# Kernel tuning notes

Hardware: AMD Instinct MI355X
Metric: run time of the kernel (lower is better)

Reference implementation:

```python
import jax, jax.numpy as jnp
import numpy as np

N, E, F, H, R, NB, G, C = 100000, 500000, 128, 64, 16, 30, 1000, 10


def setup_inputs() -> dict:
    key = jax.random.key(0)
    ks = jax.random.split(key, 12)
    s = 0.05
    x = jax.random.normal(ks[0], (N, F), jnp.float32)
    edge_index = jax.random.randint(ks[1], (2, E), 0, N, dtype=jnp.int32)
    edge_norm = jax.random.uniform(ks[2], (E,), jnp.float32)
    edge_type = jax.random.randint(ks[3], (E,), 0, R, dtype=jnp.int32)
    seq_lengths = jnp.full((G,), N // G, dtype=jnp.int32)  # 1000 graphs x 100 nodes
    return dict(
        x=x, edge_index=edge_index, edge_norm=edge_norm, edge_type=edge_type,
        seq_lengths=seq_lengths, avec=0,
        w1_rel=jax.random.normal(ks[4], (F, H), jnp.float32) * s,
        w1_root=jax.random.normal(ks[5], (F, H), jnp.float32) * s,
        b1=jnp.zeros((H,), jnp.float32),
        bases=jax.random.normal(ks[6], (NB, H, H), jnp.float32) * s,
        comp=jax.random.normal(ks[7], (R, NB), jnp.float32) * s,
        w2_root=jax.random.normal(ks[8], (H, H), jnp.float32) * s,
        b2=jnp.zeros((H,), jnp.float32),
        lin_w=jax.random.normal(ks[9], (2 * (F + H), H), jnp.float32) * s,
        lin_b=jnp.zeros((H,), jnp.float32),
        fc_w=jax.random.normal(ks[10], (H, C), jnp.float32) * s,
        fc_b=jnp.zeros((C,), jnp.float32),
    )


def reference(x, edge_index, edge_norm, edge_type, seq_lengths, avec,
              w1_rel, w1_root, b1, bases, comp, w2_root, b2,
              lin_w, lin_b, fc_w, fc_b):
    src, dst = edge_index[0], edge_index[1]

    # --- GraphConv (PyG): out_i = W_rel @ sum_{j->i} w_ji x_j + W_root x_i + b
    msg = x[src] * edge_norm[:, None]                       # [E, F]
    agg = jax.ops.segment_sum(msg, dst, num_segments=N)     # [N, F]
    h = agg @ w1_rel + x @ w1_root + b1                     # [N, H]

    # --- RGCNConv with basis decomposition, mean aggregation per relation
    W = jnp.einsum('rb,bio->rio', comp, bases)              # [R, H, H]
    hs = h[src]                                             # [E, H]
    out = h @ w2_root + b2                                  # root transform + bias
    for r in range(R):  # small fixed relation count
        m = (edge_type == r).astype(h.dtype)                # [E]
        s_r = jax.ops.segment_sum(hs * m[:, None], dst, num_segments=N)
        c_r = jax.ops.segment_sum(m, dst, num_segments=N)
        out = out + (s_r / jnp.maximum(c_r, 1.0)[:, None]) @ W[r]

    feats = jnp.concatenate([x, out], axis=-1)              # [N, F+H]

    # --- ragged per-graph sum & max pooling (replaces the Python loop)
    bounds = jnp.cumsum(seq_lengths)
    gid = jnp.searchsorted(bounds, jnp.arange(N), side='right')  # [N] graph ids
    gsum = jax.ops.segment_sum(feats, gid, num_segments=G)       # [G, F+H]
    gmax = jax.ops.segment_max(feats, gid, num_segments=G)       # [G, F+H]

    hidden = jax.nn.relu(jnp.concatenate([gsum, gmax], -1) @ lin_w + lin_b)
    # dropout is identity at inference
    logits = hidden @ fc_w + fc_b                           # [G, C]
    if avec:
        return logits
    return jax.nn.log_softmax(logits, -1)
```

## Files before the change

### kernel.cpp

```cpp
#include <hip/hip_runtime.h>
#include <hip/hip_bf16.h>

#define NN 100000
#define NE 500000
#define FD 128
#define HD 64
#define RR 16
#define NBASE 30
#define GG 1000
#define CC 10
#define NGROUP 6250

typedef __attribute__((ext_vector_type(8))) short bf16x8;
typedef __attribute__((ext_vector_type(4))) float f32x4;

__device__ inline unsigned short f2b(float x) {
  __hip_bfloat16 b = __float2bfloat16(x);
  return *reinterpret_cast<unsigned short*>(&b);
}
__device__ inline float b2f(unsigned short u) {
  return __uint_as_float(((unsigned)u) << 16);
}

__global__ void k_basis(const float* comp, const float* bases, unsigned short* Wt) {
  int idx = blockIdx.x * 256 + threadIdx.x;
  int r = idx >> 12, kj = idx & 4095;
  int k = kj >> 6, n = kj & 63;
  float acc = 0.0f;
  for (int b = 0; b < NBASE; ++b)
    acc += comp[r * NBASE + b] * bases[b * 4096 + kj];
  Wt[(r << 12) + n * 64 + k] = f2b(acc);
}

__global__ void k_wcvt(const float* w_root, const float* w_rel, const float* w2,
                       unsigned short* wcat, unsigned short* w2t) {
  int idx = blockIdx.x * 256 + threadIdx.x;
  if (idx < 16384) {
    int n = idx >> 7, k = idx & 127;
    float v = (n < 64) ? w_root[k * 64 + n] : w_rel[k * 64 + (n - 64)];
    wcat[n * 128 + k] = f2b(v);
  } else if (idx < 16384 + 4096) {
    int i2 = idx - 16384;
    int n = i2 >> 6, k = i2 & 63;
    w2t[n * 64 + k] = f2b(w2[k * 64 + n]);
  }
}

__global__ __launch_bounds__(256) void k_proj_mfma(const float* x, const unsigned short* wcat,
                                                   const float* b1, unsigned short* hroot_bf,
                                                   unsigned short* xw_bf) {
  __shared__ float red[4][64][33];
  __shared__ float ldsH[16][68];
  __shared__ unsigned short ldsX[16][72];
  int wv = threadIdx.x >> 6, l = threadIdx.x & 63, m = l & 15, q = l >> 4;
  int n0 = blockIdx.x * 16;
  const float* xr = x + (size_t)(n0 + m) * FD + wv * 32 + q * 8;
  float4 xa = *reinterpret_cast<const float4*>(xr);
  float4 xb = *reinterpret_cast<const float4*>(xr + 4);
  bf16x8 a;
  a[0] = (short)f2b(xa.x); a[1] = (short)f2b(xa.y);
  a[2] = (short)f2b(xa.z); a[3] = (short)f2b(xa.w);
  a[4] = (short)f2b(xb.x); a[5] = (short)f2b(xb.y);
  a[6] = (short)f2b(xb.z); a[7] = (short)f2b(xb.w);
  f32x4 zero = {0.0f, 0.0f, 0.0f, 0.0f};
#pragma unroll
  for (int nt = 0; nt < 8; ++nt) {
    bf16x8 b = *reinterpret_cast<const bf16x8*>(wcat + (nt * 16 + m) * 128 + wv * 32 + q * 8);
    f32x4 acc = __builtin_amdgcn_mfma_f32_16x16x32_bf16(a, b, zero, 0, 0, 0);
#pragma unroll
    for (int i = 0; i < 4; ++i) red[wv][l][nt * 4 + i] = acc[i];
  }
  __syncthreads();
#pragma unroll
  for (int t2 = 0; t2 < 2; ++t2) {
    int nt = wv * 2 + t2;
    float s0 = 0, s1 = 0, s2 = 0, s3 = 0;
#pragma unroll
    for (int w = 0; w < 4; ++w) {
      s0 += red[w][l][nt * 4 + 0];
      s1 += red[w][l][nt * 4 + 1];
      s2 += red[w][l][nt * 4 + 2];
      s3 += red[w][l][nt * 4 + 3];
    }
    if (nt < 4) {
      float bb = b1[nt * 16 + m];
      ldsH[q * 4 + 0][nt * 16 + m] = s0 + bb;
      ldsH[q * 4 + 1][nt * 16 + m] = s1 + bb;
      ldsH[q * 4 + 2][nt * 16 + m] = s2 + bb;
      ldsH[q * 4 + 3][nt * 16 + m] = s3 + bb;
    } else {
      int cc = (nt - 4) * 16 + m;
      ldsX[q * 4 + 0][cc] = f2b(s0);
      ldsX[q * 4 + 1][cc] = f2b(s1);
      ldsX[q * 4 + 2][cc] = f2b(s2);
      ldsX[q * 4 + 3][cc] = f2b(s3);
    }
  }
  __syncthreads();
  int t = threadIdx.x;
  {
    int row = t >> 4, c4 = (t & 15) * 4;
    ushort4 o;
    o.x = f2b(ldsH[row][c4 + 0]);
    o.y = f2b(ldsH[row][c4 + 1]);
    o.z = f2b(ldsH[row][c4 + 2]);
    o.w = f2b(ldsH[row][c4 + 3]);
    *reinterpret_cast<ushort4*>(&hroot_bf[(size_t)(n0 + row) * 64 + c4]) = o;
  }
  if (t < 128) {
    int row = t >> 3, c8 = (t & 7) * 8;
    uint4 v = *reinterpret_cast<const uint4*>(&ldsX[row][c8]);
    *reinterpret_cast<uint4*>(&xw_bf[(size_t)(n0 + row) * 64 + c8]) = v;
  }
}

__global__ void k_hists(const int* ei, const int* etype, int* hist1, int* hist2) {
  __shared__ int lh[RR];
  if (threadIdx.x < RR) lh[threadIdx.x] = 0;
  __syncthreads();
  for (int e = blockIdx.x * 256 + threadIdx.x; e < NE; e += gridDim.x * 256) {
    int t = etype[e];
    atomicAdd(&lh[t], 1);
    atomicAdd(&hist2[ei[NE + e] * RR + t], 1);
  }
  __syncthreads();
  if (threadIdx.x < RR) atomicAdd(&hist1[threadIdx.x], lh[threadIdx.x]);
}

__global__ void k_scan1(const int* hist1, int* offs, int* ctr1) {
  if (threadIdx.x == 0) {
    int s = 0;
    for (int r = 0; r < RR; ++r) { offs[r] = s; ctr1[r] = s; s += hist1[r]; }
    offs[RR] = s;
  }
}

__global__ void k_perm1(const int* etype, int* ctr1, int* perm1) {
  __shared__ int lcnt[RR], lbase[RR];
  if (threadIdx.x < RR) lcnt[threadIdx.x] = 0;
  __syncthreads();
  int e = blockIdx.x * 256 + threadIdx.x;
  int t = 0, rank = 0;
  bool valid = e < NE;
  if (valid) { t = etype[e]; rank = atomicAdd(&lcnt[t], 1); }
  __syncthreads();
  if (threadIdx.x < RR) {
    int n = lcnt[threadIdx.x];
    lbase[threadIdx.x] = n ? atomicAdd(&ctr1[threadIdx.x], n) : 0;
  }
  __syncthreads();
  if (valid) perm1[lbase[t] + rank] = e;
}

__device__ inline int block_scan_incl(int v, int* ps, int t) {
  ps[t] = v;
  __syncthreads();
  for (int off = 1; off < 256; off <<= 1) {
    int u = (t >= off) ? ps[t - off] : 0;
    __syncthreads();
    ps[t] += u;
    __syncthreads();
  }
  return ps[t];
}

__global__ void k_scanA(const int* hist2, int* bsum) {
  __shared__ int red[256];
  int t = threadIdx.x;
  red[t] = hist2[blockIdx.x * 256 + t];
  __syncthreads();
  for (int s = 128; s; s >>= 1) {
    if (t < s) red[t] += red[t + s];
    __syncthreads();
  }
  if (t == 0) bsum[blockIdx.x] = red[0];
}

__global__ void k_scanB(int* bsum) {
  int t = threadIdx.x;
  int loc[25];
  int s = 0;
  if (t < 250) {
    for (int i = 0; i < 25; ++i) { loc[i] = bsum[t * 25 + i]; s += loc[i]; }
  }
  __shared__ int ps[256];
  int incl = block_scan_incl(s, ps, t);
  int base = incl - s;
  if (t < 250) {
    int run = base;
    for (int i = 0; i < 25; ++i) { int tmp = loc[i]; bsum[t * 25 + i] = run; run += tmp; }
  }
}

__global__ void k_scanC(const int* hist2, const int* bsum, int* rowptr2, int* ctr2) {
  int t = threadIdx.x;
  int gid = blockIdx.x * 256 + t;
  int v = hist2[gid];
  __shared__ int ps[256];
  int incl = block_scan_incl(v, ps, t);
  int ex = bsum[blockIdx.x] + incl - v;
  rowptr2[gid] = ex;
  ctr2[gid] = ex;
}

__global__ void k_perm2(const int* perm1, const int* ei, const int* etype, const float* enorm,
                        int* ctr2, int* pos2, int* es, float* en) {
  int p = blockIdx.x * 256 + threadIdx.x;
  if (p >= NE) return;
  int e = perm1[p];
  int key = ei[NE + e] * RR + etype[e];
  int pos = atomicAdd(&ctr2[key], 1);
  pos2[p] = pos;
  es[pos] = ei[e];
  en[pos] = enorm[e];
}

__global__ __launch_bounds__(256) void k_gconv_seg(const int* rowptr2, const int* es,
    const float* en, const unsigned short* xw_bf, const unsigned short* hroot_bf,
    unsigned short* h_bf) {
  int wv = threadIdx.x >> 6, l = threadIdx.x & 63;
  int c4 = l & 15, eq = l >> 4;
  int dst = blockIdx.x * 4 + wv;
  int lo = rowptr2[dst * RR];
  int hi = (dst == NN - 1) ? NE : rowptr2[(dst + 1) * RR];
  float4 acc = {0.0f, 0.0f, 0.0f, 0.0f};
  for (int base0 = lo; base0 < hi; base0 += 64) {
    int n = min(64, hi - base0);
    int sv = 0;
    float nv = 0.0f;
    if (l < n) { sv = es[base0 + l]; nv = en[base0 + l]; }
    int k4max = (n + 3) >> 2;
    for (int k4 = 0; k4 < k4max; ++k4) {
      int eid = k4 * 4 + eq;
      int s = __shfl(sv, eid);
      float w = __shfl(nv, eid);
      if (eid < n) {
        uint2 v = *reinterpret_cast<const uint2*>(xw_bf + (size_t)s * 64 + c4 * 4);
        acc.x += b2f((unsigned short)(v.x & 0xffffu)) * w;
        acc.y += b2f((unsigned short)(v.x >> 16)) * w;
        acc.z += b2f((unsigned short)(v.y & 0xffffu)) * w;
        acc.w += b2f((unsigned short)(v.y >> 16)) * w;
      }
    }
  }
  acc.x += __shfl_xor(acc.x, 16); acc.y += __shfl_xor(acc.y, 16);
  acc.z += __shfl_xor(acc.z, 16); acc.w += __shfl_xor(acc.w, 16);
  acc.x += __shfl_xor(acc.x, 32); acc.y += __shfl_xor(acc.y, 32);
  acc.z += __shfl_xor(acc.z, 32); acc.w += __shfl_xor(acc.w, 32);
  if (l < 16) {
    uint2 hb = *reinterpret_cast<const uint2*>(hroot_bf + (size_t)dst * 64 + l * 4);
    acc.x += b2f((unsigned short)(hb.x & 0xffffu));
    acc.y += b2f((unsigned short)(hb.x >> 16));
    acc.z += b2f((unsigned short)(hb.y & 0xffffu));
    acc.w += b2f((unsigned short)(hb.y >> 16));
    ushort4 o;
    o.x = f2b(acc.x); o.y = f2b(acc.y); o.z = f2b(acc.z); o.w = f2b(acc.w);
    *reinterpret_cast<ushort4*>(h_bf + (size_t)dst * 64 + l * 4) = o;
  }
}

__global__ __launch_bounds__(256) void k_root2_mfma(const unsigned short* h_bf,
    const unsigned short* w2t, const float* b2, float* out) {
  int wv = threadIdx.x >> 6, l = threadIdx.x & 63, m = l & 15, q = l >> 4;
  int g = blockIdx.x * 4 + wv;
  if (g >= NGROUP) return;
  int n0 = g * 16;
  f32x4 acc[4];
#pragma unroll
  for (int nt = 0; nt < 4; ++nt) acc[nt] = (f32x4){0, 0, 0, 0};
#pragma unroll
  for (int s = 0; s < 2; ++s) {
    bf16x8 a = *reinterpret_cast<const bf16x8*>(h_bf + (size_t)(n0 + m) * 64 + s * 32 + q * 8);
#pragma unroll
    for (int nt = 0; nt < 4; ++nt) {
      bf16x8 b = *reinterpret_cast<const bf16x8*>(w2t + (nt * 16 + m) * 64 + s * 32 + q * 8);
      acc[nt] = __builtin_amdgcn_mfma_f32_16x16x32_bf16(a, b, acc[nt], 0, 0, 0);
    }
  }
  float b2v[4];
#pragma unroll
  for (int nt = 0; nt < 4; ++nt) b2v[nt] = b2[nt * 16 + m];
#pragma unroll
  for (int i = 0; i < 4; ++i) {
    size_t row = n0 + q * 4 + i;
#pragma unroll
    for (int nt = 0; nt < 4; ++nt)
      out[row * 64 + nt * 16 + m] = acc[nt][i] + b2v[nt];
  }
}

__global__ __launch_bounds__(256) void k_rgcn_y(const int* perm1, const int* ei,
    const int* offs, const int* pos2, const unsigned short* h_bf, const unsigned short* Wt,
    const int* hist2, unsigned short* y_bf) {
  int r = blockIdx.x;
  int lo = offs[r], hi = offs[r + 1];
  int cnt = hi - lo;
  int wv = threadIdx.x >> 6;
  int l = threadIdx.x & 63;
  int m = l & 15, q = l >> 4;
  int ngroups = (cnt + 15) / 16;
  const unsigned short* Wr = Wt + (r << 12);
  bf16x8 bfr[2][4];
#pragma unroll
  for (int s = 0; s < 2; ++s)
#pragma unroll
    for (int nt = 0; nt < 4; ++nt)
      bfr[s][nt] = *reinterpret_cast<const bf16x8*>(Wr + (nt * 16 + m) * 64 + s * 32 + q * 8);

  for (int g = blockIdx.y * 4 + wv; g < ngroups; g += gridDim.y * 4) {
    int base = lo + g * 16;
    int ne = min(16, hi - base);
    int p = base + ((m < ne) ? m : 0);
    int ed = perm1[p];
    int src = ei[ed];
    int dst = ei[NE + ed];
    int pos = pos2[p];
    float inv = 1.0f / (float)max(hist2[dst * RR + r], 1);
    f32x4 acc[4];
#pragma unroll
    for (int nt = 0; nt < 4; ++nt) acc[nt] = (f32x4){0, 0, 0, 0};
    const unsigned short* hrow = h_bf + (size_t)src * 64 + q * 8;
#pragma unroll
    for (int s = 0; s < 2; ++s) {
      bf16x8 afr = *reinterpret_cast<const bf16x8*>(hrow + s * 32);
#pragma unroll
      for (int nt = 0; nt < 4; ++nt)
        acc[nt] = __builtin_amdgcn_mfma_f32_16x16x32_bf16(afr, bfr[s][nt], acc[nt], 0, 0, 0);
    }
#pragma unroll
    for (int i = 0; i < 4; ++i) {
      int row = q * 4 + i;
      float ir = __shfl(inv, row);
      int pr = __shfl(pos, row);
      if (row < ne) {
#pragma unroll
        for (int nt = 0; nt < 4; ++nt)
          y_bf[(size_t)pr * 64 + nt * 16 + m] = f2b(acc[nt][i] * ir);
      }
    }
  }
}

__global__ __launch_bounds__(256) void k_ysum(const int* rowptr2, const unsigned short* y_bf,
                                              float* out) {
  int wv = threadIdx.x >> 6, l = threadIdx.x & 63;
  int c4 = l & 15, eq = l >> 4;
  int dst = blockIdx.x * 4 + wv;
  int lo = rowptr2[dst * RR];
  int hi = (dst == NN - 1) ? NE : rowptr2[(dst + 1) * RR];
  float4 acc = {0.0f, 0.0f, 0.0f, 0.0f};
  for (int row = lo + eq; row < hi; row += 4) {
    uint2 v = *reinterpret_cast<const uint2*>(y_bf + (size_t)row * 64 + c4 * 4);
    acc.x += b2f((unsigned short)(v.x & 0xffffu));
    acc.y += b2f((unsigned short)(v.x >> 16));
    acc.z += b2f((unsigned short)(v.y & 0xffffu));
    acc.w += b2f((unsigned short)(v.y >> 16));
  }
  acc.x += __shfl_xor(acc.x, 16); acc.y += __shfl_xor(acc.y, 16);
  acc.z += __shfl_xor(acc.z, 16); acc.w += __shfl_xor(acc.w, 16);
  acc.x += __shfl_xor(acc.x, 32); acc.y += __shfl_xor(acc.y, 32);
  acc.z += __shfl_xor(acc.z, 32); acc.w += __shfl_xor(acc.w, 32);
  if (l < 16) {
    float4* op = reinterpret_cast<float4*>(out + (size_t)dst * 64 + l * 4);
    float4 o = *op;
    o.x += acc.x; o.y += acc.y; o.z += acc.z; o.w += acc.w;
    *op = o;
  }
}

__global__ void k_bounds(const int* seq, int* bounds) {
  __shared__ int s[GG];
  for (int i = threadIdx.x; i < GG; i += 256) s[i] = seq[i];
  __syncthreads();
  if (threadIdx.x == 0) {
    int acc = 0;
    for (int g = 0; g < GG; ++g) { acc += s[g]; bounds[g] = acc; }
  }
}

__global__ __launch_bounds__(256) void k_head(const float* x, const float* outn,
    const int* bounds, const float* lin_w, const float* lin_b,
    const float* fc_w, const float* fc_b, float* dout) {
  __shared__ float4 psum[5][48], pmax[5][48];
  __shared__ float gsum[192], gmax[192];
  __shared__ float part[4][64];
  __shared__ float hid[HD], lg[CC], mred[2];
  int g = blockIdx.x, t = threadIdx.x;
  int lo = (g == 0) ? 0 : bounds[g - 1];
  int hi = bounds[g];
  int nn = hi - lo;
  if (t < 240) {
    int c4 = t % 48, ch = t / 48;
    int a = lo + (nn * ch) / 5, b = lo + (nn * (ch + 1)) / 5;
    float4 s = {0, 0, 0, 0};
    float4 mx = {-3.4e38f, -3.4e38f, -3.4e38f, -3.4e38f};
    const float* bp;
    int stride;
    if (c4 < 32) { bp = x + (size_t)a * FD + c4 * 4; stride = FD; }
    else         { bp = outn + (size_t)a * 64 + (c4 - 32) * 4; stride = 64; }
    int n = a;
    for (; n + 4 <= b; n += 4) {
      float4 v0 = *reinterpret_cast<const float4*>(bp);
      float4 v1 = *reinterpret_cast<const float4*>(bp + stride);
      float4 v2 = *reinterpret_cast<const float4*>(bp + 2 * stride);
      float4 v3 = *reinterpret_cast<const float4*>(bp + 3 * stride);
      bp += 4 * stride;
      s.x += v0.x + v1.x + v2.x + v3.x;
      s.y += v0.y + v1.y + v2.y + v3.y;
      s.z += v0.z + v1.z + v2.z + v3.z;
      s.w += v0.w + v1.w + v2.w + v3.w;
      mx.x = fmaxf(fmaxf(fmaxf(mx.x, v0.x), fmaxf(v1.x, v2.x)), v3.x);
      mx.y = fmaxf(fmaxf(fmaxf(mx.y, v0.y), fmaxf(v1.y, v2.y)), v3.y);
      mx.z = fmaxf(fmaxf(fmaxf(mx.z, v0.z), fmaxf(v1.z, v2.z)), v3.z);
      mx.w = fmaxf(fmaxf(fmaxf(mx.w, v0.w), fmaxf(v1.w, v2.w)), v3.w);
    }
    for (; n < b; ++n) {
      float4 v = *reinterpret_cast<const float4*>(bp);
      bp += stride;
      s.x += v.x; s.y += v.y; s.z += v.z; s.w += v.w;
      mx.x = fmaxf(mx.x, v.x); mx.y = fmaxf(mx.y, v.y);
      mx.z = fmaxf(mx.z, v.z); mx.w = fmaxf(mx.w, v.w);
    }
    psum[ch][c4] = s;
    pmax[ch][c4] = mx;
  }
  __syncthreads();
  if (t < 48) {
    float4 s = psum[0][t], m = pmax[0][t];
#pragma unroll
    for (int ch = 1; ch < 5; ++ch) {
      float4 ps = psum[ch][t], pm = pmax[ch][t];
      s.x += ps.x; s.y += ps.y; s.z += ps.z; s.w += ps.w;
      m.x = fmaxf(m.x, pm.x); m.y = fmaxf(m.y, pm.y);
      m.z = fmaxf(m.z, pm.z); m.w = fmaxf(m.w, pm.w);
    }
    gsum[t * 4 + 0] = s.x; gsum[t * 4 + 1] = s.y;
    gsum[t * 4 + 2] = s.z; gsum[t * 4 + 3] = s.w;
    gmax[t * 4 + 0] = m.x; gmax[t * 4 + 1] = m.y;
    gmax[t * 4 + 2] = m.z; gmax[t * 4 + 3] = m.w;
  }
  __syncthreads();
  {
    int o = t & 63, pp = t >> 6;
    float a = 0.0f;
    int k0 = pp * 96;
    for (int k = k0; k < k0 + 96; ++k) {
      float gv = (k < 192) ? gsum[k] : gmax[k - 192];
      a += gv * lin_w[k * 64 + o];
    }
    part[pp][o] = a;
  }
  __syncthreads();
  if (t < HD) {
    float a = lin_b[t] + part[0][t] + part[1][t] + part[2][t] + part[3][t];
    hid[t] = fmaxf(a, 0.0f);
  }
  __syncthreads();
  if (t < CC) {
    float a = fc_b[t];
    for (int k = 0; k < HD; ++k) a += hid[k] * fc_w[k * CC + t];
    lg[t] = a;
  }
  __syncthreads();
  if (t == 0) {
    float mm = lg[0];
#pragma unroll
    for (int i = 1; i < CC; ++i) mm = fmaxf(mm, lg[i]);
    float se = 0.0f;
#pragma unroll
    for (int i = 0; i < CC; ++i) se += __expf(lg[i] - mm);
    mred[0] = mm;
    mred[1] = __logf(se);
  }
  __syncthreads();
  if (t < CC) dout[g * CC + t] = lg[t] - mred[0] - mred[1];
}

extern "C" void kernel_launch(void* const* d_in, const int* in_sizes, int n_in,
                              void* d_out, int out_size, void* d_ws, size_t ws_size,
                              hipStream_t stream) {
  const float* x     = (const float*)d_in[0];
  const int* ei      = (const int*)d_in[1];
  const float* enorm = (const float*)d_in[2];
  const int* etype   = (const int*)d_in[3];
  const int* seq     = (const int*)d_in[4];
  const float* w1_rel  = (const float*)d_in[6];
  const float* w1_root = (const float*)d_in[7];
  const float* b1      = (const float*)d_in[8];
  const float* bases   = (const float*)d_in[9];
  const float* comp    = (const float*)d_in[10];
  const float* w2      = (const float*)d_in[11];
  const float* b2      = (const float*)d_in[12];
  const float* lin_w   = (const float*)d_in[13];
  const float* lin_b   = (const float*)d_in[14];
  const float* fc_w    = (const float*)d_in[15];
  const float* fc_b    = (const float*)d_in[16];
  float* dout = (float*)d_out;

  char* p = (char*)d_ws;
  unsigned short* hroot_bf = (unsigned short*)p; p += (size_t)NN * 64 * 2;
  unsigned short* xw_bf    = (unsigned short*)p; p += (size_t)NN * 64 * 2;
  float* out  = (float*)p;  p += (size_t)NN * 64 * 4;
  unsigned short* y_bf = (unsigned short*)p; p += (size_t)NE * 64 * 2;
  unsigned short* h_bf = (unsigned short*)p; p += (size_t)NN * 64 * 2;
  unsigned short* Wt   = (unsigned short*)p; p += (size_t)RR * 4096 * 2;
  unsigned short* wcat = (unsigned short*)p; p += (size_t)128 * 128 * 2;
  unsigned short* w2t  = (unsigned short*)p; p += (size_t)64 * 64 * 2;
  int* perm1   = (int*)p; p += (size_t)NE * 4;
  int* pos2    = (int*)p; p += (size_t)NE * 4;
  int* es      = (int*)p; p += (size_t)NE * 4;
  float* en    = (float*)p; p += (size_t)NE * 4;
  int* hist2   = (int*)p; p += (size_t)NN * RR * 4;
  int* rowptr2 = (int*)p; p += (size_t)NN * RR * 4;
  int* bsum    = (int*)p; p += (size_t)NGROUP * 4;
  int* hist1   = (int*)p; p += 64;
  int* ctr1    = (int*)p; p += 64;
  int* offs    = (int*)p; p += 68;
  int* bounds  = (int*)p; p += (size_t)GG * 4;
  int* ctr2    = (int*)out;

  hipMemsetAsync(hist2, 0, (size_t)NN * RR * 4, stream);
  hipMemsetAsync(hist1, 0, 128, stream);

  hipLaunchKernelGGL(k_basis, dim3(256), dim3(256), 0, stream, comp, bases, Wt);
  hipLaunchKernelGGL(k_wcvt, dim3(80), dim3(256), 0, stream, w1_root, w1_rel, w2, wcat, w2t);
  hipLaunchKernelGGL(k_proj_mfma, dim3(NGROUP), dim3(256), 0, stream, x, wcat, b1,
                     hroot_bf, xw_bf);
  hipLaunchKernelGGL(k_hists, dim3(512), dim3(256), 0, stream, ei, etype, hist1, hist2);
  hipLaunchKernelGGL(k_scan1, dim3(1), dim3(64), 0, stream, hist1, offs, ctr1);
  hipLaunchKernelGGL(k_perm1, dim3((NE + 255) / 256), dim3(256), 0, stream, etype, ctr1, perm1);
  hipLaunchKernelGGL(k_scanA, dim3(NGROUP), dim3(256), 0, stream, hist2, bsum);
  hipLaunchKernelGGL(k_scanB, dim3(1), dim3(256), 0, stream, bsum);
  hipLaunchKernelGGL(k_scanC, dim3(NGROUP), dim3(256), 0, stream, hist2, bsum, rowptr2, ctr2);
  hipLaunchKernelGGL(k_perm2, dim3((NE + 255) / 256), dim3(256), 0, stream,
                     perm1, ei, etype, enorm, ctr2, pos2, es, en);
  hipLaunchKernelGGL(k_gconv_seg, dim3(NN / 4), dim3(256), 0, stream,
                     rowptr2, es, en, xw_bf, hroot_bf, h_bf);
  hipLaunchKernelGGL(k_root2_mfma, dim3((NGROUP + 3) / 4), dim3(256), 0, stream,
                     h_bf, w2t, b2, out);
  hipLaunchKernelGGL(k_rgcn_y, dim3(RR, 128), dim3(256), 0, stream,
                     perm1, ei, offs, pos2, h_bf, Wt, hist2, y_bf);
  hipLaunchKernelGGL(k_ysum, dim3(NN / 4), dim3(256), 0, stream, rowptr2, y_bf, out);
  hipLaunchKernelGGL(k_bounds, dim3(1), dim3(256), 0, stream, seq, bounds);
  hipLaunchKernelGGL(k_head, dim3(GG), dim3(256), 0, stream, x, out, bounds,
                     lin_w, lin_b, fc_w, fc_b, dout);
}
```

Before: 391.5 us.

## Fuse root transform into y-sum, precompute edge src/inv, restructure projection GEMM

Merges the separate root-GEMM kernel into the per-destination y-sum kernel, so the output is written once instead of written and then read-modify-written. The edge permutation kernel now stores each edge's source and inverse relation count in permuted order, which removes the dependent gathers in the RGCN message kernel. The input projection is reworked so each wave does the full K loop for its own 16-row tile with accumulators kept in registers, dropping the cross-wave LDS reduction. The cost is more per-wave register pressure and two extra edge arrays to write.

```diff
diff --git a/kernel.cpp b/kernel.cpp
--- a/kernel.cpp
+++ b/kernel.cpp
@@ -49,68 +49,54 @@
 __global__ __launch_bounds__(256) void k_proj_mfma(const float* x, const unsigned short* wcat,
                                                    const float* b1, unsigned short* hroot_bf,
                                                    unsigned short* xw_bf) {
-  __shared__ float red[4][64][33];
-  __shared__ float ldsH[16][68];
-  __shared__ unsigned short ldsX[16][72];
+  __shared__ unsigned short ldsO[4][16][72];
   int wv = threadIdx.x >> 6, l = threadIdx.x & 63, m = l & 15, q = l >> 4;
-  int n0 = blockIdx.x * 16;
-  const float* xr = x + (size_t)(n0 + m) * FD + wv * 32 + q * 8;
-  float4 xa = *reinterpret_cast<const float4*>(xr);
-  float4 xb = *reinterpret_cast<const float4*>(xr + 4);
-  bf16x8 a;
-  a[0] = (short)f2b(xa.x); a[1] = (short)f2b(xa.y);
-  a[2] = (short)f2b(xa.z); a[3] = (short)f2b(xa.w);
-  a[4] = (short)f2b(xb.x); a[5] = (short)f2b(xb.y);
-  a[6] = (short)f2b(xb.z); a[7] = (short)f2b(xb.w);
-  f32x4 zero = {0.0f, 0.0f, 0.0f, 0.0f};
-#pragma unroll
-  for (int nt = 0; nt < 8; ++nt) {
-    bf16x8 b = *reinterpret_cast<const bf16x8*>(wcat + (nt * 16 + m) * 128 + wv * 32 + q * 8);
-    f32x4 acc = __builtin_amdgcn_mfma_f32_16x16x32_bf16(a, b, zero, 0, 0, 0);
-#pragma unroll
-    for (int i = 0; i < 4; ++i) red[wv][l][nt * 4 + i] = acc[i];
-  }
-  __syncthreads();
-#pragma unroll
-  for (int t2 = 0; t2 < 2; ++t2) {
-    int nt = wv * 2 + t2;
-    float s0 = 0, s1 = 0, s2 = 0, s3 = 0;
-#pragma unroll
-    for (int w = 0; w < 4; ++w) {
-      s0 += red[w][l][nt * 4 + 0];
-      s1 += red[w][l][nt * 4 + 1];
-      s2 += red[w][l][nt * 4 + 2];
-      s3 += red[w][l][nt * 4 + 3];
-    }
-    if (nt < 4) {
-      float bb = b1[nt * 16 + m];
-      ldsH[q * 4 + 0][nt * 16 + m] = s0 + bb;
-      ldsH[q * 4 + 1][nt * 16 + m] = s1 + bb;
-      ldsH[q * 4 + 2][nt * 16 + m] = s2 + bb;
-      ldsH[q * 4 + 3][nt * 16 + m] = s3 + bb;
-    } else {
-      int cc = (nt - 4) * 16 + m;
-      ldsX[q * 4 + 0][cc] = f2b(s0);
-      ldsX[q * 4 + 1][cc] = f2b(s1);
-      ldsX[q * 4 + 2][cc] = f2b(s2);
-      ldsX[q * 4 + 3][cc] = f2b(s3);
-    }
-  }
-  __syncthreads();
-  int t = threadIdx.x;
-  {
-    int row = t >> 4, c4 = (t & 15) * 4;
-    ushort4 o;
-    o.x = f2b(ldsH[row][c4 + 0]);
-    o.y = f2b(ldsH[row][c4 + 1]);
-    o.z = f2b(ldsH[row][c4 + 2]);
-    o.w = f2b(ldsH[row][c4 + 3]);
-    *reinterpret_cast<ushort4*>(&hroot_bf[(size_t)(n0 + row) * 64 + c4]) = o;
-  }
-  if (t < 128) {
-    int row = t >> 3, c8 = (t & 7) * 8;
-    uint4 v = *reinterpret_cast<const uint4*>(&ldsX[row][c8]);
-    *reinterpret_cast<uint4*>(&xw_bf[(size_t)(n0 + row) * 64 + c8]) = v;
+  int g = blockIdx.x * 4 + wv;
+  bool act = g < NGROUP;
+  size_t n0 = (size_t)g * 16;
+  f32x4 acc[8];
+#pragma unroll
+  for (int nt = 0; nt < 8; ++nt) acc[nt] = (f32x4){0, 0, 0, 0};
+  if (act) {
+#pragma unroll
+    for (int s = 0; s < 4; ++s) {
+      const float* xr = x + (n0 + m) * FD + s * 32 + q * 8;
+      float4 xa = *reinterpret_cast<const float4*>(xr);
+      float4 xb = *reinterpret_cast<const float4*>(xr + 4);
+      bf16x8 a;
+      a[0] = (short)f2b(xa.x); a[1] = (short)f2b(xa.y);
+      a[2] = (short)f2b(xa.z); a[3] = (short)f2b(xa.w);
+      a[4] = (short)f2b(xb.x); a[5] = (short)f2b(xb.y);
+      a[6] = (short)f2b(xb.z); a[7] = (short)f2b(xb.w);
+#pragma unroll
+      for (int nt = 0; nt < 8; ++nt) {
+        bf16x8 b = *reinterpret_cast<const bf16x8*>(wcat + (nt * 16 + m) * 128 + s * 32 + q * 8);
+        acc[nt] = __builtin_amdgcn_mfma_f32_16x16x32_bf16(a, b, acc[nt], 0, 0, 0);
+      }
+    }
+  }
+  float b1v[4];
+#pragma unroll
+  for (int nt = 0; nt < 4; ++nt) b1v[nt] = b1[nt * 16 + m];
+#pragma unroll
+  for (int half = 0; half < 2; ++half) {
+#pragma unroll
+    for (int nt = 0; nt < 4; ++nt)
+#pragma unroll
+      for (int i = 0; i < 4; ++i) {
+        float v = acc[half * 4 + nt][i] + (half == 0 ? b1v[nt] : 0.0f);
+        ldsO[wv][q * 4 + i][nt * 16 + m] = f2b(v);
+      }
+    __syncthreads();
+    unsigned short* dstbuf = half == 0 ? hroot_bf : xw_bf;
+#pragma unroll
+    for (int h2 = 0; h2 < 2; ++h2) {
+      int row = h2 * 8 + (l >> 3), ch = l & 7;
+      uint4 v = *reinterpret_cast<const uint4*>(&ldsO[wv][row][ch * 8]);
+      if (act)
+        *reinterpret_cast<uint4*>(&dstbuf[(n0 + row) * 64 + ch * 8]) = v;
+    }
+    __syncthreads();
   }
 }
 
@@ -204,15 +190,19 @@
 }
 
 __global__ void k_perm2(const int* perm1, const int* ei, const int* etype, const float* enorm,
-                        int* ctr2, int* pos2, int* es, float* en) {
+                        const int* hist2, int* ctr2, int* pos2, int* es, float* en,
+                        int* ts, float* tinv) {
   int p = blockIdx.x * 256 + threadIdx.x;
   if (p >= NE) return;
   int e = perm1[p];
+  int src = ei[e];
   int key = ei[NE + e] * RR + etype[e];
   int pos = atomicAdd(&ctr2[key], 1);
   pos2[p] = pos;
-  es[pos] = ei[e];
+  es[pos] = src;
   en[pos] = enorm[e];
+  ts[p] = src;
+  tinv[p] = 1.0f / (float)max(hist2[key], 1);
 }
 
 __global__ __launch_bounds__(256) void k_gconv_seg(const int* rowptr2, const int* es,
@@ -259,39 +249,9 @@
   }
 }
 
-__global__ __launch_bounds__(256) void k_root2_mfma(const unsigned short* h_bf,
-    const unsigned short* w2t, const float* b2, float* out) {
-  int wv = threadIdx.x >> 6, l = threadIdx.x & 63, m = l & 15, q = l >> 4;
-  int g = blockIdx.x * 4 + wv;
-  if (g >= NGROUP) return;
-  int n0 = g * 16;
-  f32x4 acc[4];
-#pragma unroll
-  for (int nt = 0; nt < 4; ++nt) acc[nt] = (f32x4){0, 0, 0, 0};
-#pragma unroll
-  for (int s = 0; s < 2; ++s) {
-    bf16x8 a = *reinterpret_cast<const bf16x8*>(h_bf + (size_t)(n0 + m) * 64 + s * 32 + q * 8);
-#pragma unroll
-    for (int nt = 0; nt < 4; ++nt) {
-      bf16x8 b = *reinterpret_cast<const bf16x8*>(w2t + (nt * 16 + m) * 64 + s * 32 + q * 8);
-      acc[nt] = __builtin_amdgcn_mfma_f32_16x16x32_bf16(a, b, acc[nt], 0, 0, 0);
-    }
-  }
-  float b2v[4];
-#pragma unroll
-  for (int nt = 0; nt < 4; ++nt) b2v[nt] = b2[nt * 16 + m];
-#pragma unroll
-  for (int i = 0; i < 4; ++i) {
-    size_t row = n0 + q * 4 + i;
-#pragma unroll
-    for (int nt = 0; nt < 4; ++nt)
-      out[row * 64 + nt * 16 + m] = acc[nt][i] + b2v[nt];
-  }
-}
-
-__global__ __launch_bounds__(256) void k_rgcn_y(const int* perm1, const int* ei,
-    const int* offs, const int* pos2, const unsigned short* h_bf, const unsigned short* Wt,
-    const int* hist2, unsigned short* y_bf) {
+__global__ __launch_bounds__(256) void k_rgcn_y(const int* ts, const float* tinv,
+    const int* pos2, const int* offs, const unsigned short* h_bf, const unsigned short* Wt,
+    unsigned short* y_bf) {
   int r = blockIdx.x;
   int lo = offs[r], hi = offs[r + 1];
   int cnt = hi - lo;
@@ -311,11 +271,9 @@
     int base = lo + g * 16;
     int ne = min(16, hi - base);
     int p = base + ((m < ne) ? m : 0);
-    int ed = perm1[p];
-    int src = ei[ed];
-    int dst = ei[NE + ed];
+    int src = ts[p];
     int pos = pos2[p];
-    float inv = 1.0f / (float)max(hist2[dst * RR + r], 1);
+    float inv = tinv[p];
     f32x4 acc[4];
 #pragma unroll
     for (int nt = 0; nt < 4; ++nt) acc[nt] = (f32x4){0, 0, 0, 0};
@@ -341,31 +299,46 @@
   }
 }
 
-__global__ __launch_bounds__(256) void k_ysum(const int* rowptr2, const unsigned short* y_bf,
-                                              float* out) {
+__global__ __launch_bounds__(256) void k_out(const int* rowptr2, const unsigned short* y_bf,
+    const unsigned short* h_bf, const unsigned short* w2t, const float* b2, float* out) {
+  __shared__ float ldsC[16][68];
   int wv = threadIdx.x >> 6, l = threadIdx.x & 63;
   int c4 = l & 15, eq = l >> 4;
-  int dst = blockIdx.x * 4 + wv;
-  int lo = rowptr2[dst * RR];
-  int hi = (dst == NN - 1) ? NE : rowptr2[(dst + 1) * RR];
-  float4 acc = {0.0f, 0.0f, 0.0f, 0.0f};
-  for (int row = lo + eq; row < hi; row += 4) {
-    uint2 v = *reinterpret_cast<const uint2*>(y_bf + (size_t)row * 64 + c4 * 4);
-    acc.x += b2f((unsigned short)(v.x & 0xffffu));
-    acc.y += b2f((unsigned short)(v.x >> 16));
-    acc.z += b2f((unsigned short)(v.y & 0xffffu));
-    acc.w += b2f((unsigned short)(v.y >> 16));
-  }
-  acc.x += __shfl_xor(acc.x, 16); acc.y += __shfl_xor(acc.y, 16);
-  acc.z += __shfl_xor(acc.z, 16); acc.w += __shfl_xor(acc.w, 16);
-  acc.x += __shfl_xor(acc.x, 32); acc.y += __shfl_xor(acc.y, 32);
-  acc.z += __shfl_xor(acc.z, 32); acc.w += __shfl_xor(acc.w, 32);
-  if (l < 16) {
-    float4* op = reinterpret_cast<float4*>(out + (size_t)dst * 64 + l * 4);
-    float4 o = *op;
-    o.x += acc.x; o.y += acc.y; o.z += acc.z; o.w += acc.w;
-    *op = o;
-  }
+  size_t d0 = (size_t)blockIdx.x * 16;
+  for (int dd = 0; dd < 4; ++dd) {
+    int dst = (int)d0 + wv * 4 + dd;
+    int lo = rowptr2[dst * RR];
+    int hi = (dst == NN - 1) ? NE : rowptr2[(dst + 1) * RR];
+    float4 acc = {0.0f, 0.0f, 0.0f, 0.0f};
+    for (int row = lo + eq; row < hi; row += 4) {
+      uint2 v = *reinterpret_cast<const uint2*>(y_bf + (size_t)row * 64 + c4 * 4);
+      acc.x += b2f((unsigned short)(v.x & 0xffffu));
+      acc.y += b2f((unsigned short)(v.x >> 16));
+      acc.z += b2f((unsigned short)(v.y & 0xffffu));
+      acc.w += b2f((unsigned short)(v.y >> 16));
+    }
+    acc.x += __shfl_xor(acc.x, 16); acc.y += __shfl_xor(acc.y, 16);
+    acc.z += __shfl_xor(acc.z, 16); acc.w += __shfl_xor(acc.w, 16);
+    acc.x += __shfl_xor(acc.x, 32); acc.y += __shfl_xor(acc.y, 32);
+    acc.z += __shfl_xor(acc.z, 32); acc.w += __shfl_xor(acc.w, 32);
+    if (l < 16)
+      *reinterpret_cast<float4*>(&ldsC[wv * 4 + dd][l * 4]) = acc;
+  }
+  __syncthreads();
+  int m = l & 15, q = l >> 4, nt = wv;
+  float bb = b2[nt * 16 + m];
+  f32x4 acc;
+#pragma unroll
+  for (int i = 0; i < 4; ++i) acc[i] = ldsC[q * 4 + i][nt * 16 + m] + bb;
+#pragma unroll
+  for (int s = 0; s < 2; ++s) {
+    bf16x8 a = *reinterpret_cast<const bf16x8*>(h_bf + (d0 + m) * 64 + s * 32 + q * 8);
+    bf16x8 b = *reinterpret_cast<const bf16x8*>(w2t + (nt * 16 + m) * 64 + s * 32 + q * 8);
+    acc = __builtin_amdgcn_mfma_f32_16x16x32_bf16(a, b, acc, 0, 0, 0);
+  }
+#pragma unroll
+  for (int i = 0; i < 4; ++i)
+    out[(d0 + q * 4 + i) * 64 + nt * 16 + m] = acc[i];
 }
 
 __global__ void k_bounds(const int* seq, int* bounds) {
@@ -510,6 +483,8 @@
   int* pos2    = (int*)p; p += (size_t)NE * 4;
   int* es      = (int*)p; p += (size_t)NE * 4;
   float* en    = (float*)p; p += (size_t)NE * 4;
+  int* ts      = (int*)p; p += (size_t)NE * 4;
+  float* tinv  = (float*)p; p += (size_t)NE * 4;
   int* hist2   = (int*)p; p += (size_t)NN * RR * 4;
   int* rowptr2 = (int*)p; p += (size_t)NN * RR * 4;
   int* bsum    = (int*)p; p += (size_t)NGROUP * 4;
@@ -524,7 +499,7 @@
 
   hipLaunchKernelGGL(k_basis, dim3(256), dim3(256), 0, stream, comp, bases, Wt);
   hipLaunchKernelGGL(k_wcvt, dim3(80), dim3(256), 0, stream, w1_root, w1_rel, w2, wcat, w2t);
-  hipLaunchKernelGGL(k_proj_mfma, dim3(NGROUP), dim3(256), 0, stream, x, wcat, b1,
+  hipLaunchKernelGGL(k_proj_mfma, dim3((NGROUP + 3) / 4), dim3(256), 0, stream, x, wcat, b1,
                      hroot_bf, xw_bf);
   hipLaunchKernelGGL(k_hists, dim3(512), dim3(256), 0, stream, ei, etype, hist1, hist2);
   hipLaunchKernelGGL(k_scan1, dim3(1), dim3(64), 0, stream, hist1, offs, ctr1);
@@ -533,14 +508,13 @@
   hipLaunchKernelGGL(k_scanB, dim3(1), dim3(256), 0, stream, bsum);
   hipLaunchKernelGGL(k_scanC, dim3(NGROUP), dim3(256), 0, stream, hist2, bsum, rowptr2, ctr2);
   hipLaunchKernelGGL(k_perm2, dim3((NE + 255) / 256), dim3(256), 0, stream,
-                     perm1, ei, etype, enorm, ctr2, pos2, es, en);
+                     perm1, ei, etype, enorm, hist2, ctr2, pos2, es, en, ts, tinv);
   hipLaunchKernelGGL(k_gconv_seg, dim3(NN / 4), dim3(256), 0, stream,
                      rowptr2, es, en, xw_bf, hroot_bf, h_bf);
-  hipLaunchKernelGGL(k_root2_mfma, dim3((NGROUP + 3) / 4), dim3(256), 0, stream,
-                     h_bf, w2t, b2, out);
   hipLaunchKernelGGL(k_rgcn_y, dim3(RR, 128), dim3(256), 0, stream,
-                     perm1, ei, offs, pos2, h_bf, Wt, hist2, y_bf);
-  hipLaunchKernelGGL(k_ysum, dim3(NN / 4), dim3(256), 0, stream, rowptr2, y_bf, out);
+                     ts, tinv, pos2, offs, h_bf, Wt, y_bf);
+  hipLaunchKernelGGL(k_out, dim3(NN / 16), dim3(256), 0, stream,
+                     rowptr2, y_bf, h_bf, w2t, b2, out);
   hipLaunchKernelGGL(k_bounds, dim3(1), dim3(256), 0, stream, seq, bounds);
   hipLaunchKernelGGL(k_head, dim3(GG), dim3(256), 0, stream, x, out, bounds,
                      lin_w, lin_b, fc_w, fc_b, dout);
```

Measured after the change: 384.8 us. No clear change (-1.7%).
